# Optimization experiments

Hardware: AMD Instinct MI355X
Metric: run time of the kernel (lower is better)

Reference implementation:

```python
import jax, jax.numpy as jnp
import numpy as np

N, D, H = 2048, 64, 64  # num_nodes, in_channels, hidden_channels


def setup_inputs() -> dict:
    key = jax.random.key(0)
    k0, k1, k2 = jax.random.split(key, 3)
    z = jax.random.normal(k0, (N, D), dtype=jnp.float32)
    # torch.nn.Linear params: W [out, in], y = x @ W.T + b
    W1 = jax.random.normal(k1, (H, 2 * D), dtype=jnp.float32) * (1.0 / np.sqrt(2 * D)).astype(np.float32)
    b1 = jnp.zeros((H,), dtype=jnp.float32)
    W2 = jax.random.normal(k2, (1, H), dtype=jnp.float32) * (1.0 / np.sqrt(H)).astype(np.float32)
    b2 = jnp.zeros((1,), dtype=jnp.float32)
    return {"z": z, "W1": W1, "b1": b1, "W2": W2, "b2": b2}


def reference(z, W1, b1, W2, b2):
    # decode(): adj[i, j] = Linear2(relu(Linear1(cat(z[i], z[j]))))  (dropout off: eval mode)
    # Efficient form: split W1 so cat(z_i, z_j) @ W1.T = z_i @ Wa.T + z_j @ Wb.T,
    # avoiding materializing the [N, N, 2D] concat tensor.
    n, d = z.shape
    Wa, Wb = W1[:, :d], W1[:, d:]           # each [H, D]
    hi = z @ Wa.T                            # [N, H] contribution from row node i
    hj = z @ Wb.T                            # [N, H] contribution from col node j
    h = jax.nn.relu(hi[:, None, :] + hj[None, :, :] + b1)  # [N, N, H]
    adj = jnp.einsum('ijh,h->ij', h, W2[0]) + b2[0]         # [N, N]
    # self_loop_mask=True: zero out the diagonal after sigmoid
    probs = jax.nn.sigmoid(adj) * (1.0 - jnp.eye(n, dtype=adj.dtype))
    return probs
```

## Files before the change

kernel.cpp:

```cpp
#include <hip/hip_runtime.h>
#include <math.h>

#define NN 2048
#define DD 64
#define HH 64
#define TILE 128
#define TP (TILE + 4)

__global__ __launch_bounds__(256) void prep_kernel(
    const float* __restrict__ z, const float* __restrict__ W1,
    const float* __restrict__ b1, const float* __restrict__ W2,
    float* __restrict__ u, float* __restrict__ v,
    float* __restrict__ a, float* __restrict__ b) {
  __shared__ float zs[8 * DD];
  const int t = threadIdx.x;
  const int i0 = blockIdx.x * 8;
  if (t < 128) {
    reinterpret_cast<float4*>(zs)[t] =
        reinterpret_cast<const float4*>(z + (size_t)i0 * DD)[t];
  }
  __syncthreads();

  const int hs = t & 127;
  const int rg = t >> 7;
  const int h = hs & 63;
  const int side = hs >> 6;
  const float* wrow = W1 + h * (2 * DD) + side * DD;

  float acc0 = 0.f, acc1 = 0.f, acc2 = 0.f, acc3 = 0.f;
#pragma unroll
  for (int d4 = 0; d4 < DD / 4; ++d4) {
    const float4 wv = reinterpret_cast<const float4*>(wrow)[d4];
    const float* z0 = zs + (rg * 4 + 0) * DD + d4 * 4;
    const float* z1 = z0 + DD;
    const float* z2 = z1 + DD;
    const float* z3 = z2 + DD;
    acc0 = fmaf(z0[3], wv.w, fmaf(z0[2], wv.z, fmaf(z0[1], wv.y, fmaf(z0[0], wv.x, acc0))));
    acc1 = fmaf(z1[3], wv.w, fmaf(z1[2], wv.z, fmaf(z1[1], wv.y, fmaf(z1[0], wv.x, acc1))));
    acc2 = fmaf(z2[3], wv.w, fmaf(z2[2], wv.z, fmaf(z2[1], wv.y, fmaf(z2[0], wv.x, acc2))));
    acc3 = fmaf(z3[3], wv.w, fmaf(z3[2], wv.z, fmaf(z3[1], wv.y, fmaf(z3[0], wv.x, acc3))));
  }
  const float bias = side ? 0.0f : b1[h];
  const float s0 = acc0 + bias, s1 = acc1 + bias, s2 = acc2 + bias, s3 = acc3 + bias;
  float* dst = side ? v : u;
  const int ib = i0 + rg * 4;
  dst[(size_t)(ib + 0) * HH + h] = s0;
  dst[(size_t)(ib + 1) * HH + h] = s1;
  dst[(size_t)(ib + 2) * HH + h] = s2;
  dst[(size_t)(ib + 3) * HH + h] = s3;

  const float wh = W2[h];
  float r0 = wh * s0, r1 = wh * s1, r2 = wh * s2, r3 = wh * s3;
#pragma unroll
  for (int m = 1; m < 64; m <<= 1) {
    r0 += __shfl_xor(r0, m);
    r1 += __shfl_xor(r1, m);
    r2 += __shfl_xor(r2, m);
    r3 += __shfl_xor(r3, m);
  }
  if ((t & 63) == 0) {
    float* d2 = side ? b : a;
    d2[ib + 0] = 0.5f * r0;
    d2[ib + 1] = 0.5f * r1;
    d2[ib + 2] = 0.5f * r2;
    d2[ib + 3] = 0.5f * r3;
  }
}

__global__ __launch_bounds__(512, 2) void pair_kernel(
    const float* __restrict__ u, const float* __restrict__ v,
    const float* __restrict__ a, const float* __restrict__ b,
    const float* __restrict__ W2, const float* __restrict__ b2,
    float* __restrict__ out) {
  __shared__ float su[HH][TP];
  __shared__ float sv[HH][TP];

  const int t = threadIdx.x;
  const int i0 = blockIdx.y * TILE;
  const int j0 = blockIdx.x * TILE;

  {
    const int r = t >> 4;
    const int c = t & 15;
    const float* us = u + (size_t)(i0 + 4 * r) * HH + 4 * c;
    const float4 a0 = *reinterpret_cast<const float4*>(us);
    const float4 a1 = *reinterpret_cast<const float4*>(us + HH);
    const float4 a2 = *reinterpret_cast<const float4*>(us + 2 * HH);
    const float4 a3 = *reinterpret_cast<const float4*>(us + 3 * HH);
    *reinterpret_cast<float4*>(&su[4 * c + 0][4 * r]) = make_float4(a0.x, a1.x, a2.x, a3.x);
    *reinterpret_cast<float4*>(&su[4 * c + 1][4 * r]) = make_float4(a0.y, a1.y, a2.y, a3.y);
    *reinterpret_cast<float4*>(&su[4 * c + 2][4 * r]) = make_float4(a0.z, a1.z, a2.z, a3.z);
    *reinterpret_cast<float4*>(&su[4 * c + 3][4 * r]) = make_float4(a0.w, a1.w, a2.w, a3.w);
    const float* vs = v + (size_t)(j0 + 4 * r) * HH + 4 * c;
    const float4 c0 = *reinterpret_cast<const float4*>(vs);
    const float4 c1 = *reinterpret_cast<const float4*>(vs + HH);
    const float4 c2 = *reinterpret_cast<const float4*>(vs + 2 * HH);
    const float4 c3 = *reinterpret_cast<const float4*>(vs + 3 * HH);
    *reinterpret_cast<float4*>(&sv[4 * c + 0][4 * r]) = make_float4(c0.x, c1.x, c2.x, c3.x);
    *reinterpret_cast<float4*>(&sv[4 * c + 1][4 * r]) = make_float4(c0.y, c1.y, c2.y, c3.y);
    *reinterpret_cast<float4*>(&sv[4 * c + 2][4 * r]) = make_float4(c0.z, c1.z, c2.z, c3.z);
    *reinterpret_cast<float4*>(&sv[4 * c + 3][4 * r]) = make_float4(c0.w, c1.w, c2.w, c3.w);
  }
  __syncthreads();

  const int tx = t & 15;
  const int ty = t >> 4;

  float acc[4][8] = {};
#pragma unroll 4
  for (int h = 0; h < HH; ++h) {
    const float wh = W2[h];
    const float4 ua = *reinterpret_cast<const float4*>(&su[h][ty * 4]);
    const float4 vb0 = *reinterpret_cast<const float4*>(&sv[h][tx * 8]);
    const float4 vb1 = *reinterpret_cast<const float4*>(&sv[h][tx * 8 + 4]);
    const float uav[4] = {ua.x, ua.y, ua.z, ua.w};
    const float vbv[8] = {vb0.x, vb0.y, vb0.z, vb0.w, vb1.x, vb1.y, vb1.z, vb1.w};
#pragma unroll
    for (int k = 0; k < 4; ++k) {
#pragma unroll
      for (int cc = 0; cc < 8; ++cc) {
        acc[k][cc] = fmaf(wh, fabsf(uav[k] + vbv[cc]), acc[k][cc]);
      }
    }
  }

  const float bias2 = b2[0];
  const float4 bj0 = *reinterpret_cast<const float4*>(b + j0 + tx * 8);
  const float4 bj1 = *reinterpret_cast<const float4*>(b + j0 + tx * 8 + 4);
  const float bj[8] = {bj0.x, bj0.y, bj0.z, bj0.w, bj1.x, bj1.y, bj1.z, bj1.w};

#pragma unroll
  for (int k = 0; k < 4; ++k) {
    const int i = i0 + ty * 4 + k;
    const float ai = a[i];
    float r[8];
#pragma unroll
    for (int cc = 0; cc < 8; ++cc) {
      const float x = ai + bj[cc] + bias2 + 0.5f * acc[k][cc];
      const float sg = 1.0f / (1.0f + __expf(-x));
      r[cc] = (i == j0 + tx * 8 + cc) ? 0.0f : sg;
    }
    float* orow = out + (size_t)i * NN + j0 + tx * 8;
    *reinterpret_cast<float4*>(orow) = make_float4(r[0], r[1], r[2], r[3]);
    *reinterpret_cast<float4*>(orow + 4) = make_float4(r[4], r[5], r[6], r[7]);
  }
}

extern "C" void kernel_launch(void* const* d_in, const int* in_sizes, int n_in,
                              void* d_out, int out_size, void* d_ws, size_t ws_size,
                              hipStream_t stream) {
  const float* z  = (const float*)d_in[0];
  const float* W1 = (const float*)d_in[1];
  const float* b1 = (const float*)d_in[2];
  const float* W2 = (const float*)d_in[3];
  const float* b2 = (const float*)d_in[4];
  float* out = (float*)d_out;

  float* u = (float*)d_ws;
  float* v = u + (size_t)NN * HH;
  float* a = v + (size_t)NN * HH;
  float* b = a + NN;

  prep_kernel<<<NN / 8, 256, 0, stream>>>(z, W1, b1, W2, u, v, a, b);
  pair_kernel<<<dim3(NN / TILE, NN / TILE), 512, 0, stream>>>(u, v, a, b, W2, b2, out);
}
```

Measured before the change: 92.39 us.

## Restructure pair kernel: v columns in registers, u rows broadcast from LDS

Reworks the pair kernel tiling to 32x256 tiles with 256 threads. Each lane now holds four v rows directly in registers, loaded from global memory, while u values are read from LDS as wave-uniform broadcasts. The intent is to cut LDS traffic and bank conflicts in the inner loop and to use more blocks (512 instead of 256) for better occupancy. The cost is uncoalesced strided global loads of v (each lane reads its own row) and scalar output stores instead of float4 stores.

```diff
diff --git a/kernel.cpp b/kernel.cpp
--- a/kernel.cpp
+++ b/kernel.cpp
@@ -4,8 +4,6 @@
 #define NN 2048
 #define DD 64
 #define HH 64
-#define TILE 128
-#define TP (TILE + 4)
 
 __global__ __launch_bounds__(256) void prep_kernel(
     const float* __restrict__ z, const float* __restrict__ W1,
@@ -67,19 +65,18 @@
   }
 }
 
-__global__ __launch_bounds__(512, 2) void pair_kernel(
+__global__ __launch_bounds__(256, 2) void pair_kernel(
     const float* __restrict__ u, const float* __restrict__ v,
     const float* __restrict__ a, const float* __restrict__ b,
     const float* __restrict__ W2, const float* __restrict__ b2,
     float* __restrict__ out) {
-  __shared__ float su[HH][TP];
-  __shared__ float sv[HH][TP];
+  __shared__ float su[HH][36];
 
   const int t = threadIdx.x;
-  const int i0 = blockIdx.y * TILE;
-  const int j0 = blockIdx.x * TILE;
+  const int i0 = blockIdx.y * 32;
+  const int j0 = blockIdx.x * 256;
 
-  {
+  if (t < 128) {
     const int r = t >> 4;
     const int c = t & 15;
     const float* us = u + (size_t)(i0 + 4 * r) * HH + 4 * c;
@@ -91,58 +88,80 @@
     *reinterpret_cast<float4*>(&su[4 * c + 1][4 * r]) = make_float4(a0.y, a1.y, a2.y, a3.y);
     *reinterpret_cast<float4*>(&su[4 * c + 2][4 * r]) = make_float4(a0.z, a1.z, a2.z, a3.z);
     *reinterpret_cast<float4*>(&su[4 * c + 3][4 * r]) = make_float4(a0.w, a1.w, a2.w, a3.w);
-    const float* vs = v + (size_t)(j0 + 4 * r) * HH + 4 * c;
-    const float4 c0 = *reinterpret_cast<const float4*>(vs);
-    const float4 c1 = *reinterpret_cast<const float4*>(vs + HH);
-    const float4 c2 = *reinterpret_cast<const float4*>(vs + 2 * HH);
-    const float4 c3 = *reinterpret_cast<const float4*>(vs + 3 * HH);
-    *reinterpret_cast<float4*>(&sv[4 * c + 0][4 * r]) = make_float4(c0.x, c1.x, c2.x, c3.x);
-    *reinterpret_cast<float4*>(&sv[4 * c + 1][4 * r]) = make_float4(c0.y, c1.y, c2.y, c3.y);
-    *reinterpret_cast<float4*>(&sv[4 * c + 2][4 * r]) = make_float4(c0.z, c1.z, c2.z, c3.z);
-    *reinterpret_cast<float4*>(&sv[4 * c + 3][4 * r]) = make_float4(c0.w, c1.w, c2.w, c3.w);
   }
   __syncthreads();
 
-  const int tx = t & 15;
-  const int ty = t >> 4;
+  const int L = t & 63;
+  const int w = t >> 6;
+  const int ib = w * 8;
 
-  float acc[4][8] = {};
-#pragma unroll 4
-  for (int h = 0; h < HH; ++h) {
-    const float wh = W2[h];
-    const float4 ua = *reinterpret_cast<const float4*>(&su[h][ty * 4]);
-    const float4 vb0 = *reinterpret_cast<const float4*>(&sv[h][tx * 8]);
-    const float4 vb1 = *reinterpret_cast<const float4*>(&sv[h][tx * 8 + 4]);
-    const float uav[4] = {ua.x, ua.y, ua.z, ua.w};
-    const float vbv[8] = {vb0.x, vb0.y, vb0.z, vb0.w, vb1.x, vb1.y, vb1.z, vb1.w};
+  const float* vr0 = v + (size_t)(j0 + L) * HH;
+  const float* vr1 = v + (size_t)(j0 + 64 + L) * HH;
+  const float* vr2 = v + (size_t)(j0 + 128 + L) * HH;
+  const float* vr3 = v + (size_t)(j0 + 192 + L) * HH;
+
+  float acc[8][4] = {};
+  for (int hc = 0; hc < 8; ++hc) {
+    const float4 wq0 = *reinterpret_cast<const float4*>(W2 + hc * 8);
+    const float4 wq1 = *reinterpret_cast<const float4*>(W2 + hc * 8 + 4);
+    const float wa[8] = {wq0.x, wq0.y, wq0.z, wq0.w, wq1.x, wq1.y, wq1.z, wq1.w};
+    const float4 v00 = *reinterpret_cast<const float4*>(vr0 + hc * 8);
+    const float4 v01 = *reinterpret_cast<const float4*>(vr0 + hc * 8 + 4);
+    const float4 v10 = *reinterpret_cast<const float4*>(vr1 + hc * 8);
+    const float4 v11 = *reinterpret_cast<const float4*>(vr1 + hc * 8 + 4);
+    const float4 v20 = *reinterpret_cast<const float4*>(vr2 + hc * 8);
+    const float4 v21 = *reinterpret_cast<const float4*>(vr2 + hc * 8 + 4);
+    const float4 v30 = *reinterpret_cast<const float4*>(vr3 + hc * 8);
+    const float4 v31 = *reinterpret_cast<const float4*>(vr3 + hc * 8 + 4);
+    const float vc0[8] = {v00.x, v00.y, v00.z, v00.w, v01.x, v01.y, v01.z, v01.w};
+    const float vc1[8] = {v10.x, v10.y, v10.z, v10.w, v11.x, v11.y, v11.z, v11.w};
+    const float vc2[8] = {v20.x, v20.y, v20.z, v20.w, v21.x, v21.y, v21.z, v21.w};
+    const float vc3[8] = {v30.x, v30.y, v30.z, v30.w, v31.x, v31.y, v31.z, v31.w};
 #pragma unroll
-    for (int k = 0; k < 4; ++k) {
+    for (int hh = 0; hh < 8; ++hh) {
+      const float wh = wa[hh];
+      const float* sr = &su[hc * 8 + hh][ib];
+      const float4 q0 = *reinterpret_cast<const float4*>(sr);
+      const float4 q1 = *reinterpret_cast<const float4*>(sr + 4);
+      const float uu[8] = {q0.x, q0.y, q0.z, q0.w, q1.x, q1.y, q1.z, q1.w};
+      const float t0 = vc0[hh], t1 = vc1[hh], t2 = vc2[hh], t3 = vc3[hh];
 #pragma unroll
-      for (int cc = 0; cc < 8; ++cc) {
-        acc[k][cc] = fmaf(wh, fabsf(uav[k] + vbv[cc]), acc[k][cc]);
+      for (int m = 0; m < 8; ++m) {
+        acc[m][0] = fmaf(wh, fabsf(uu[m] + t0), acc[m][0]);
+        acc[m][1] = fmaf(wh, fabsf(uu[m] + t1), acc[m][1]);
+        acc[m][2] = fmaf(wh, fabsf(uu[m] + t2), acc[m][2]);
+        acc[m][3] = fmaf(wh, fabsf(uu[m] + t3), acc[m][3]);
       }
     }
   }
 
   const float bias2 = b2[0];
-  const float4 bj0 = *reinterpret_cast<const float4*>(b + j0 + tx * 8);
-  const float4 bj1 = *reinterpret_cast<const float4*>(b + j0 + tx * 8 + 4);
-  const float bj[8] = {bj0.x, bj0.y, bj0.z, bj0.w, bj1.x, bj1.y, bj1.z, bj1.w};
+  const float bj0 = b[j0 + L];
+  const float bj1 = b[j0 + 64 + L];
+  const float bj2 = b[j0 + 128 + L];
+  const float bj3 = b[j0 + 192 + L];
 
 #pragma unroll
-  for (int k = 0; k < 4; ++k) {
-    const int i = i0 + ty * 4 + k;
-    const float ai = a[i];
-    float r[8];
-#pragma unroll
-    for (int cc = 0; cc < 8; ++cc) {
-      const float x = ai + bj[cc] + bias2 + 0.5f * acc[k][cc];
-      const float sg = 1.0f / (1.0f + __expf(-x));
-      r[cc] = (i == j0 + tx * 8 + cc) ? 0.0f : sg;
-    }
-    float* orow = out + (size_t)i * NN + j0 + tx * 8;
-    *reinterpret_cast<float4*>(orow) = make_float4(r[0], r[1], r[2], r[3]);
-    *reinterpret_cast<float4*>(orow + 4) = make_float4(r[4], r[5], r[6], r[7]);
+  for (int m = 0; m < 8; ++m) {
+    const int i = i0 + ib + m;
+    const float ai = a[i] + bias2;
+    const float x0 = ai + bj0 + 0.5f * acc[m][0];
+    const float x1 = ai + bj1 + 0.5f * acc[m][1];
+    const float x2 = ai + bj2 + 0.5f * acc[m][2];
+    const float x3 = ai + bj3 + 0.5f * acc[m][3];
+    float r0 = 1.0f / (1.0f + __expf(-x0));
+    float r1 = 1.0f / (1.0f + __expf(-x1));
+    float r2 = 1.0f / (1.0f + __expf(-x2));
+    float r3 = 1.0f / (1.0f + __expf(-x3));
+    if (i == j0 + L) r0 = 0.0f;
+    if (i == j0 + 64 + L) r1 = 0.0f;
+    if (i == j0 + 128 + L) r2 = 0.0f;
+    if (i == j0 + 192 + L) r3 = 0.0f;
+    float* orow = out + (size_t)i * NN;
+    orow[j0 + L] = r0;
+    orow[j0 + 64 + L] = r1;
+    orow[j0 + 128 + L] = r2;
+    orow[j0 + 192 + L] = r3;
   }
 }
 
@@ -162,5 +181,5 @@
   float* b = a + NN;
 
   prep_kernel<<<NN / 8, 256, 0, stream>>>(z, W1, b1, W2, u, v, a, b);
-  pair_kernel<<<dim3(NN / TILE, NN / TILE), 512, 0, stream>>>(u, v, a, b, W2, b2, out);
+  pair_kernel<<<dim3(NN / 256, NN / 32), 256, 0, stream>>>(u, v, a, b, W2, b2, out);
 }
```

After: 95.55 us. 1.03x slower.

## Replace shared-memory tiling with register/readlane broadcast and transposed v layout

Applied to the files above, without the earlier changes.

The pair kernel no longer stages u and v tiles in LDS. Each wave holds four rows of u in registers and broadcasts each hidden element with readlane. The v matrix is now written transposed by the prep kernel so each lane can load float4 columns straight from global memory. Removing LDS traffic and the barrier is meant to cut load/store overhead in the inner loop. In exchange each thread computes a smaller 4x4 tile, so more loads per FMA go to global/L2, and the readlanes add scalar work.

```diff
diff --git a/kernel.cpp b/kernel.cpp
--- a/kernel.cpp
+++ b/kernel.cpp
@@ -4,13 +4,11 @@
 #define NN 2048
 #define DD 64
 #define HH 64
-#define TILE 128
-#define TP (TILE + 4)
 
 __global__ __launch_bounds__(256) void prep_kernel(
     const float* __restrict__ z, const float* __restrict__ W1,
     const float* __restrict__ b1, const float* __restrict__ W2,
-    float* __restrict__ u, float* __restrict__ v,
+    float* __restrict__ u, float* __restrict__ vt,
     float* __restrict__ a, float* __restrict__ b) {
   __shared__ float zs[8 * DD];
   const int t = threadIdx.x;
@@ -42,12 +40,16 @@
   }
   const float bias = side ? 0.0f : b1[h];
   const float s0 = acc0 + bias, s1 = acc1 + bias, s2 = acc2 + bias, s3 = acc3 + bias;
-  float* dst = side ? v : u;
   const int ib = i0 + rg * 4;
-  dst[(size_t)(ib + 0) * HH + h] = s0;
-  dst[(size_t)(ib + 1) * HH + h] = s1;
-  dst[(size_t)(ib + 2) * HH + h] = s2;
-  dst[(size_t)(ib + 3) * HH + h] = s3;
+  if (side) {
+    float* vrow = vt + (size_t)h * NN + ib;
+    vrow[0] = s0; vrow[1] = s1; vrow[2] = s2; vrow[3] = s3;
+  } else {
+    u[(size_t)(ib + 0) * HH + h] = s0;
+    u[(size_t)(ib + 1) * HH + h] = s1;
+    u[(size_t)(ib + 2) * HH + h] = s2;
+    u[(size_t)(ib + 3) * HH + h] = s3;
+  }
 
   const float wh = W2[h];
   float r0 = wh * s0, r1 = wh * s1, r2 = wh * s2, r3 = wh * s3;
@@ -67,82 +69,65 @@
   }
 }
 
-__global__ __launch_bounds__(512, 2) void pair_kernel(
-    const float* __restrict__ u, const float* __restrict__ v,
+__global__ __launch_bounds__(256, 4) void pair_kernel(
+    const float* __restrict__ u, const float* __restrict__ vt,
     const float* __restrict__ a, const float* __restrict__ b,
     const float* __restrict__ W2, const float* __restrict__ b2,
     float* __restrict__ out) {
-  __shared__ float su[HH][TP];
-  __shared__ float sv[HH][TP];
+  const int t = threadIdx.x;
+  const int L = t & 63;
+  const int w = t >> 6;
+  const int i0 = blockIdx.y * 16 + w * 4;
+  const int j0 = blockIdx.x * 256;
+  const int jL = j0 + 4 * L;
 
-  const int t = threadIdx.x;
-  const int i0 = blockIdx.y * TILE;
-  const int j0 = blockIdx.x * TILE;
+  float ur[4];
+#pragma unroll
+  for (int m = 0; m < 4; ++m) ur[m] = u[(size_t)(i0 + m) * HH + L];
 
-  {
-    const int r = t >> 4;
-    const int c = t & 15;
-    const float* us = u + (size_t)(i0 + 4 * r) * HH + 4 * c;
-    const float4 a0 = *reinterpret_cast<const float4*>(us);
-    const float4 a1 = *reinterpret_cast<const float4*>(us + HH);
-    const float4 a2 = *reinterpret_cast<const float4*>(us + 2 * HH);
-    const float4 a3 = *reinterpret_cast<const float4*>(us + 3 * HH);
-    *reinterpret_cast<float4*>(&su[4 * c + 0][4 * r]) = make_float4(a0.x, a1.x, a2.x, a3.x);
-    *reinterpret_cast<float4*>(&su[4 * c + 1][4 * r]) = make_float4(a0.y, a1.y, a2.y, a3.y);
-    *reinterpret_cast<float4*>(&su[4 * c + 2][4 * r]) = make_float4(a0.z, a1.z, a2.z, a3.z);
-    *reinterpret_cast<float4*>(&su[4 * c + 3][4 * r]) = make_float4(a0.w, a1.w, a2.w, a3.w);
-    const float* vs = v + (size_t)(j0 + 4 * r) * HH + 4 * c;
-    const float4 c0 = *reinterpret_cast<const float4*>(vs);
-    const float4 c1 = *reinterpret_cast<const float4*>(vs + HH);
-    const float4 c2 = *reinterpret_cast<const float4*>(vs + 2 * HH);
-    const float4 c3 = *reinterpret_cast<const float4*>(vs + 3 * HH);
-    *reinterpret_cast<float4*>(&sv[4 * c + 0][4 * r]) = make_float4(c0.x, c1.x, c2.x, c3.x);
-    *reinterpret_cast<float4*>(&sv[4 * c + 1][4 * r]) = make_float4(c0.y, c1.y, c2.y, c3.y);
-    *reinterpret_cast<float4*>(&sv[4 * c + 2][4 * r]) = make_float4(c0.z, c1.z, c2.z, c3.z);
-    *reinterpret_cast<float4*>(&sv[4 * c + 3][4 * r]) = make_float4(c0.w, c1.w, c2.w, c3.w);
-  }
-  __syncthreads();
+  const float4* vt4 = reinterpret_cast<const float4*>(vt);
+  const int vcol = (j0 >> 2) + L;
 
-  const int tx = t & 15;
-  const int ty = t >> 4;
-
-  float acc[4][8] = {};
-#pragma unroll 4
-  for (int h = 0; h < HH; ++h) {
-    const float wh = W2[h];
-    const float4 ua = *reinterpret_cast<const float4*>(&su[h][ty * 4]);
-    const float4 vb0 = *reinterpret_cast<const float4*>(&sv[h][tx * 8]);
-    const float4 vb1 = *reinterpret_cast<const float4*>(&sv[h][tx * 8 + 4]);
-    const float uav[4] = {ua.x, ua.y, ua.z, ua.w};
-    const float vbv[8] = {vb0.x, vb0.y, vb0.z, vb0.w, vb1.x, vb1.y, vb1.z, vb1.w};
+  float acc[4][4] = {};
 #pragma unroll
-    for (int k = 0; k < 4; ++k) {
+  for (int hc = 0; hc < 8; ++hc) {
+    float4 q[8];
 #pragma unroll
-      for (int cc = 0; cc < 8; ++cc) {
-        acc[k][cc] = fmaf(wh, fabsf(uav[k] + vbv[cc]), acc[k][cc]);
+    for (int hh = 0; hh < 8; ++hh)
+      q[hh] = vt4[(size_t)(hc * 8 + hh) * (NN / 4) + vcol];
+#pragma unroll
+    for (int hh = 0; hh < 8; ++hh) {
+      const int h = hc * 8 + hh;
+      const float wh = W2[h];
+#pragma unroll
+      for (int m = 0; m < 4; ++m) {
+        const float um = __int_as_float(
+            __builtin_amdgcn_readlane(__float_as_int(ur[m]), h));
+        acc[m][0] = fmaf(wh, fabsf(um + q[hh].x), acc[m][0]);
+        acc[m][1] = fmaf(wh, fabsf(um + q[hh].y), acc[m][1]);
+        acc[m][2] = fmaf(wh, fabsf(um + q[hh].z), acc[m][2]);
+        acc[m][3] = fmaf(wh, fabsf(um + q[hh].w), acc[m][3]);
       }
     }
   }
 
   const float bias2 = b2[0];
-  const float4 bj0 = *reinterpret_cast<const float4*>(b + j0 + tx * 8);
-  const float4 bj1 = *reinterpret_cast<const float4*>(b + j0 + tx * 8 + 4);
-  const float bj[8] = {bj0.x, bj0.y, bj0.z, bj0.w, bj1.x, bj1.y, bj1.z, bj1.w};
+  const float4 bj = *reinterpret_cast<const float4*>(b + jL);
+  const float bjv[4] = {bj.x, bj.y, bj.z, bj.w};
 
 #pragma unroll
-  for (int k = 0; k < 4; ++k) {
-    const int i = i0 + ty * 4 + k;
-    const float ai = a[i];
-    float r[8];
+  for (int m = 0; m < 4; ++m) {
+    const int i = i0 + m;
+    const float ai = a[i] + bias2;
+    float r[4];
 #pragma unroll
-    for (int cc = 0; cc < 8; ++cc) {
-      const float x = ai + bj[cc] + bias2 + 0.5f * acc[k][cc];
-      const float sg = 1.0f / (1.0f + __expf(-x));
-      r[cc] = (i == j0 + tx * 8 + cc) ? 0.0f : sg;
+    for (int c = 0; c < 4; ++c) {
+      const float x = ai + bjv[c] + 0.5f * acc[m][c];
+      r[c] = 1.0f / (1.0f + __expf(-x));
+      if (i == jL + c) r[c] = 0.0f;
     }
-    float* orow = out + (size_t)i * NN + j0 + tx * 8;
-    *reinterpret_cast<float4*>(orow) = make_float4(r[0], r[1], r[2], r[3]);
-    *reinterpret_cast<float4*>(orow + 4) = make_float4(r[4], r[5], r[6], r[7]);
+    *reinterpret_cast<float4*>(out + (size_t)i * NN + jL) =
+        make_float4(r[0], r[1], r[2], r[3]);
   }
 }
 
@@ -156,11 +141,11 @@
   const float* b2 = (const float*)d_in[4];
   float* out = (float*)d_out;
 
-  float* u = (float*)d_ws;
-  float* v = u + (size_t)NN * HH;
-  float* a = v + (size_t)NN * HH;
-  float* b = a + NN;
+  float* u  = (float*)d_ws;
+  float* vt = u + (size_t)NN * HH;
+  float* a  = vt + (size_t)NN * HH;
+  float* b  = a + NN;
 
-  prep_kernel<<<NN / 8, 256, 0, stream>>>(z, W1, b1, W2, u, v, a, b);
-  pair_kernel<<<dim3(NN / TILE, NN / TILE), 512, 0, stream>>>(u, v, a, b, W2, b2, out);
+  prep_kernel<<<NN / 8, 256, 0, stream>>>(z, W1, b1, W2, u, vt, a, b);
+  pair_kernel<<<dim3(NN / 256, NN / 16), 256, 0, stream>>>(u, vt, a, b, W2, b2, out);
 }
```

Result: no change. 91.14 us (-1.4%).
